# Kernel optimization log

Hardware: AMD Instinct MI355X
Metric: run time of the kernel (lower is better)

Reference implementation:

```python
import jax, jax.numpy as jnp
import numpy as np

N = 50000        # nodes
R = 51           # enriched relations (25 fwd + 25 inverse + self-loop)
F_IN = 32        # feat_size
E = 32           # embed_size
C = 16           # num_classes
B = 30           # num_bases
NNZ = 2_000_000  # nonzeros in vertical adjacency


def _xavier(key, shape):
    # mimics nn.init.xavier_uniform_ with gain for relu (sqrt(2))
    fan_in, fan_out = shape[-2], shape[-1]
    a = np.sqrt(2.0) * np.sqrt(6.0 / (fan_in + fan_out))
    return jax.random.uniform(key, shape, jnp.float32, -a, a)


def setup_inputs() -> dict:
    key = jax.random.key(0)
    ks = jax.random.split(key, 8)
    # COO of vertical adjacency, shape (R*N, N)
    rows = jax.random.randint(ks[0], (NNZ,), 0, R * N)
    cols = jax.random.randint(ks[1], (NNZ,), 0, N)
    # row-normalized values: vals = 1 / row_degree  (sum_sparse with rows=True)
    deg = jax.ops.segment_sum(jnp.ones((NNZ,), jnp.float32), rows, num_segments=R * N)
    vals = (1.0 / jnp.maximum(deg, 1.0))[rows]
    features = jax.random.normal(ks[2], (N, F_IN), jnp.float32)
    comps1 = _xavier(ks[3], (R, B))
    bases1 = _xavier(ks[4], (B, F_IN, E))
    comps2 = _xavier(ks[5], (R, B))
    bases2 = _xavier(ks[6], (B, E, C))
    bias1 = jnp.zeros((E,), jnp.float32)
    bias2 = jnp.zeros((C,), jnp.float32)
    return {
        "features": features, "vals": vals,
        "comps1": comps1, "bases1": bases1, "bias1": bias1,
        "comps2": comps2, "bases2": bases2, "bias2": bias2,
        "rows": rows, "cols": cols,
    }


def _spmm(rows, cols, vals, x):
    # (R*N, N) sparse @ (N, f) dense -> (R*N, f)
    return jax.ops.segment_sum(vals[:, None] * x[cols], rows, num_segments=R * N)


def reference(features, vals, comps1, bases1, bias1, comps2, bases2, bias2, rows, cols):
    # layer 1: SpMM then basis-decomposed per-relation mixing
    h = _spmm(rows, cols, vals, features).reshape(R, N, F_IN)   # (r, n, f)
    w1 = jnp.einsum('rb,bfe->rfe', comps1, bases1)              # (r, f, e)
    h = jnp.einsum('rnf,rfe->ne', h, w1)                        # (n, e)
    h = jax.nn.relu(h + bias1)
    # layer 2
    h = _spmm(rows, cols, vals, h).reshape(R, N, E)             # (r, n, e)
    w2 = jnp.einsum('rb,bho->rho', comps2, bases2)              # (r, e, c)
    h = jnp.einsum('rho,rnh->no', w2, h)                        # (n, c)
    return h + bias2
```

## Files before the change

kernel.cpp:

```cpp
#include <hip/hip_runtime.h>

#define NNODES 50000
#define RREL 51
#define FIN 32
#define EDIM 32
#define CDIM 16
#define BB 30
#define NNZ_ 2000000
#define EPB 4096
#define NBUK 391
#define PCAP_MAX 2750128

typedef unsigned int uint32;
typedef unsigned short ushort;
typedef uint32 u32x2 __attribute__((ext_vector_type(2)));
typedef uint32 u32x4 __attribute__((ext_vector_type(4)));
typedef short bf16x8 __attribute__((ext_vector_type(8)));
typedef float f32x4 __attribute__((ext_vector_type(4)));
typedef float f32x16 __attribute__((ext_vector_type(16)));

static __device__ __forceinline__ uint32 pack_bf16x2(float a, float b) {
    uint32 ua = __builtin_bit_cast(uint32, a);
    uint32 ub = __builtin_bit_cast(uint32, b);
    ua += 0x7fffu + ((ua >> 16) & 1u);
    ub += 0x7fffu + ((ub >> 16) & 1u);
    return (ua >> 16) | (ub & 0xffff0000u);
}
static __device__ __forceinline__ ushort bf16_1(float x) {
    uint32 u = __builtin_bit_cast(uint32, x);
    u += 0x7fffu + ((u >> 16) & 1u);
    return (ushort)(u >> 16);
}

__global__ void k_weights2(const float* __restrict__ bases1, const float* __restrict__ bases2,
                           ushort* __restrict__ Wb1, ushort* __restrict__ Wb2) {
    int i = blockIdx.x * 256 + threadIdx.x;
    if (i < 960 * 32) {
        int e = i & 31, k = i >> 5;
        int b = k >> 5, f = k & 31;
        float v = bases1[b * 1024 + f * 32 + e];
        Wb1[((k >> 3) * 32 + e) * 8 + (k & 7)] = bf16_1(v);
    }
    if (i < 960 * 16) {
        int e = i & 15, k = i >> 4;
        int b = k >> 5, h = k & 31;
        float v = bases2[b * 512 + h * 16 + e];
        Wb2[((k >> 3) * 16 + e) * 8 + (k & 7)] = bf16_1(v);
    }
}

__global__ void k_tobf16(const float2* __restrict__ src, uint32* __restrict__ dst, int n2) {
    int i = blockIdx.x * 256 + threadIdx.x;
    if (i < n2) {
        float2 f = src[i];
        dst[i] = pack_bf16x2(f.x, f.y);
    }
}

__global__ __launch_bounds__(1024) void k_bukhist(const int* __restrict__ rows,
                                                  int* __restrict__ buk_cnt) {
    __shared__ int lc[NBUK];
    int t = threadIdx.x;
    if (t < NBUK) lc[t] = 0;
    __syncthreads();
    size_t k = (size_t)blockIdx.x * EPB + (size_t)t * 4;
    int rr[4];
    if (k + 4 <= NNZ_) {
        int4 rw = *(const int4*)(rows + k);
        rr[0] = rw.x; rr[1] = rw.y; rr[2] = rw.z; rr[3] = rw.w;
    } else {
#pragma unroll
        for (int j = 0; j < 4; j++) rr[j] = (k + j < NNZ_) ? rows[k + j] : -1;
    }
#pragma unroll
    for (int j = 0; j < 4; j++)
        if (rr[j] >= 0) {
            int rel = rr[j] / NNODES;
            int dst = rr[j] - rel * NNODES;
            atomicAdd(&lc[dst >> 7], 1);
        }
    __syncthreads();
    if (t < NBUK) atomicAdd(&buk_cnt[t], lc[t]);
}

__global__ void k_scan1(const int* __restrict__ buk_cnt, int* __restrict__ buk_base,
                        int* __restrict__ buk_cur) {
    if (threadIdx.x == 0) {
        int a = 0;
        for (int b = 0; b < NBUK; b++) { buk_base[b] = a; buk_cur[b] = a; a += buk_cnt[b]; }
        buk_base[NBUK] = a;
    }
}

__global__ __launch_bounds__(1024) void k_bucket2(const int* __restrict__ rows,
                                                  const int* __restrict__ cols,
                                                  const float* __restrict__ vals,
                                                  int* __restrict__ buk_cur,
                                                  u32x2* __restrict__ tok8,
                                                  float* __restrict__ sval_b) {
    __shared__ int bukc[NBUK], lb[NBUK], gb[NBUK];
    __shared__ int ssum[1024];
    __shared__ u32x2 st8[EPB];
    __shared__ float sv[EPB];
    int t = threadIdx.x;
    size_t base = (size_t)blockIdx.x * EPB;
    int total = (int)(((size_t)NNZ_ - base < (size_t)EPB) ? ((size_t)NNZ_ - base) : (size_t)EPB);
    if (t < NBUK) bukc[t] = 0;
    __syncthreads();
    size_t k = base + (size_t)t * 4;
    int bv[4]; uint32 tx[4], ty[4]; float vv[4];
    if (k + 4 <= NNZ_) {
        int4 rw = *(const int4*)(rows + k);
        int4 cw = *(const int4*)(cols + k);
        float4 vw = *(const float4*)(vals + k);
        int rr[4] = {rw.x, rw.y, rw.z, rw.w};
        int cc[4] = {cw.x, cw.y, cw.z, cw.w};
        vv[0] = vw.x; vv[1] = vw.y; vv[2] = vw.z; vv[3] = vw.w;
#pragma unroll
        for (int j = 0; j < 4; j++) {
            int rel = rr[j] / NNODES;
            int dst = rr[j] - rel * NNODES;
            bv[j] = dst >> 7;
            tx[j] = (uint32)dst | ((uint32)rel << 16);
            ty[j] = (uint32)cc[j] | ((uint32)rel << 16);
        }
    } else {
#pragma unroll
        for (int j = 0; j < 4; j++) {
            if (k + j < NNZ_) {
                int r = rows[k + j];
                int rel = r / NNODES;
                int dst = r - rel * NNODES;
                bv[j] = dst >> 7;
                tx[j] = (uint32)dst | ((uint32)rel << 16);
                ty[j] = (uint32)cols[k + j] | ((uint32)rel << 16);
                vv[j] = vals[k + j];
            } else bv[j] = -1;
        }
    }
#pragma unroll
    for (int j = 0; j < 4; j++)
        if (bv[j] >= 0) atomicAdd(&bukc[bv[j]], 1);
    __syncthreads();
    int v = (t < NBUK) ? bukc[t] : 0;
    ssum[t] = v;
    __syncthreads();
    for (int off = 1; off < 1024; off <<= 1) {
        int u = (t >= off) ? ssum[t - off] : 0;
        __syncthreads();
        ssum[t] += u;
        __syncthreads();
    }
    if (t < NBUK) { lb[t] = ssum[t] - v; gb[t] = atomicAdd(&buk_cur[t], v); }
    __syncthreads();
    if (t < NBUK) bukc[t] = 0;
    __syncthreads();
#pragma unroll
    for (int j = 0; j < 4; j++) {
        if (bv[j] >= 0) {
            int slot = lb[bv[j]] + atomicAdd(&bukc[bv[j]], 1);
            u32x2 w; w.x = tx[j]; w.y = ty[j];
            st8[slot] = w;
            sv[slot] = vv[j];
        }
    }
    __syncthreads();
    for (int s = t; s < total; s += 1024) {
        u32x2 w = st8[s];
        int bk = (int)((w.x & 0xFFFFu) >> 7);
        int pos = gb[bk] + (s - lb[bk]);
        tok8[pos] = w;
        sval_b[pos] = sv[s];
    }
}

__global__ __launch_bounds__(256) void k_rank3a(const u32x2* __restrict__ tok8,
                                                const int* __restrict__ buk_base,
                                                int* __restrict__ pbuk_cnt) {
    __shared__ int lcnt[128];
    __shared__ int tot;
    int b = blockIdx.x, t = threadIdx.x;
    if (t < 128) lcnt[t] = 0;
    if (t == 0) tot = 0;
    __syncthreads();
    int lo = buk_base[b], hi = buk_base[b + 1];
    for (int i = lo + t; i < hi; i += 256) atomicAdd(&lcnt[tok8[i].x & 127], 1);
    __syncthreads();
    if (t < 128) atomicAdd(&tot, (lcnt[t] + 15) & ~15);
    __syncthreads();
    if (t == 0) pbuk_cnt[b] = tot;
}

__global__ void k_scan2(const int* __restrict__ pbuk_cnt, int* __restrict__ pbuk_base) {
    if (threadIdx.x == 0) {
        int a = 0;
        for (int b = 0; b < NBUK; b++) { pbuk_base[b] = a; a += pbuk_cnt[b]; }
        pbuk_base[NBUK] = a;
    }
}

__global__ __launch_bounds__(256) void k_place(const u32x2* __restrict__ tok8,
                                               const float* __restrict__ sval_b,
                                               const int* __restrict__ buk_base,
                                               const int* __restrict__ pbuk_base,
                                               int* __restrict__ pdst_base,
                                               uint32* __restrict__ pe_sr,
                                               float* __restrict__ pe_val) {
    __shared__ int lcnt[128], lexc[128], lrank[128], ssc[128];
    int b = blockIdx.x, t = threadIdx.x;
    int lo = buk_base[b], hi = buk_base[b + 1], pb = pbuk_base[b];
    if (t < 128) { lcnt[t] = 0; lrank[t] = 0; }
    __syncthreads();
    for (int i = lo + t; i < hi; i += 256) atomicAdd(&lcnt[tok8[i].x & 127], 1);
    __syncthreads();
    int v = 0;
    if (t < 128) { v = (lcnt[t] + 15) & ~15; ssc[t] = v; }
    __syncthreads();
    for (int off = 1; off < 128; off <<= 1) {
        int u = (t >= off && t < 128) ? ssc[t - off] : 0;
        __syncthreads();
        if (t < 128) ssc[t] += u;
        __syncthreads();
    }
    if (t < 128) {
        lexc[t] = ssc[t] - v;
        int d = (b << 7) + t;
        if (d <= NNODES) pdst_base[d] = pb + lexc[t];
    }
    __syncthreads();
    for (int i = lo + t; i < hi; i += 256) {
        u32x2 w = tok8[i];
        int dl = (int)(w.x & 127u);
        int pos = pb + lexc[dl] + atomicAdd(&lrank[dl], 1);
        pe_sr[pos] = w.y;
        pe_val[pos] = sval_b[i];
    }
    if (t < 128) {
        int s0 = pb + lexc[t] + lcnt[t];
        int s1 = pb + lexc[t] + ((lcnt[t] + 15) & ~15);
        for (int i = s0; i < s1; i++) { pe_sr[i] = 0u; pe_val[i] = 0.f; }
    }
}

template <int FO, bool RELU, bool BF16OUT>
__global__ __launch_bounds__(256) void k_fused(const uint32* __restrict__ pe_sr,
                                               const float* __restrict__ pe_val,
                                               const int* __restrict__ pdst_base,
                                               const u32x4* __restrict__ Xb,
                                               const u32x4* __restrict__ Wb,
                                               const float* __restrict__ comps,
                                               const float* __restrict__ bias,
                                               void* __restrict__ outp) {
    __shared__ ushort comps_lb[RREL * 32];
    __shared__ uint32 eds[4][64];
    __shared__ float edv[4][64];
    __shared__ __align__(16) ushort xst[4][4][512];
    __shared__ __align__(16) ushort ubuf[4][4][968];
    int t = threadIdx.x, lane = t & 63, wv = t >> 6;
    for (int i = t; i < RREL * 32; i += 256) {
        int r = i >> 5, b = i & 31;
        comps_lb[i] = (b < BB) ? bf16_1(comps[r * BB + b]) : (ushort)0;
    }
    __syncthreads();
    int m = lane & 31, hf = lane >> 5, k0 = hf * 8;
    int ln15 = lane & 15, quad = lane >> 4;
    int d0 = (blockIdx.x * 4 + wv) * 8;
    if (d0 >= NNODES) return;

    auto ccprep = [&](int wi) -> u32x4 {
        float cc[8];
#pragma unroll
        for (int j = 0; j < 8; j++) {
            uint32 sr = eds[wv][wi * 16 + k0 + j];
            float vv = edv[wv][wi * 16 + k0 + j];
            uint32 cu = (uint32)comps_lb[((sr >> 16) << 5) | m] << 16;
            cc[j] = vv * __builtin_bit_cast(float, cu);
        }
        u32x4 r = { pack_bf16x2(cc[0], cc[1]), pack_bf16x2(cc[2], cc[3]),
                    pack_bf16x2(cc[4], cc[5]), pack_bf16x2(cc[6], cc[7]) };
        return r;
    };
    auto dowin = [&](int wi, u32x4 avq, f32x16 a) -> f32x16 {
        const ushort* xs = &xst[wv][wi][0];
        uint32 b0 = (uint32)xs[(k0 + 0) * 32 + m] | ((uint32)xs[(k0 + 1) * 32 + m] << 16);
        uint32 b1 = (uint32)xs[(k0 + 2) * 32 + m] | ((uint32)xs[(k0 + 3) * 32 + m] << 16);
        uint32 b2 = (uint32)xs[(k0 + 4) * 32 + m] | ((uint32)xs[(k0 + 5) * 32 + m] << 16);
        uint32 b3 = (uint32)xs[(k0 + 6) * 32 + m] | ((uint32)xs[(k0 + 7) * 32 + m] << 16);
        u32x4 bvq = { b0, b1, b2, b3 };
        return __builtin_amdgcn_mfma_f32_32x32x16_bf16(
            __builtin_bit_cast(bf16x8, avq), __builtin_bit_cast(bf16x8, bvq), a, 0, 0, 0);
    };

    int base0 = pdst_base[d0];
    uint32 pvs = __builtin_nontemporal_load(&pe_sr[base0 + lane]);
    float  pvv = __builtin_nontemporal_load(&pe_val[base0 + lane]);
    u32x4 gx0, gx1, gx2, gx3;
    {
        int s0_ = __shfl((int)pvs, (lane >> 2), 64);
        gx0 = Xb[(size_t)((uint32)s0_ & 0xFFFFu) * 4 + (lane & 3)];
        int s1_ = __shfl((int)pvs, 16 + (lane >> 2), 64);
        gx1 = Xb[(size_t)((uint32)s1_ & 0xFFFFu) * 4 + (lane & 3)];
        int s2_ = __shfl((int)pvs, 32 + (lane >> 2), 64);
        gx2 = Xb[(size_t)((uint32)s2_ & 0xFFFFu) * 4 + (lane & 3)];
        int s3_ = __shfl((int)pvs, 48 + (lane >> 2), 64);
        gx3 = Xb[(size_t)((uint32)s3_ & 0xFFFFu) * 4 + (lane & 3)];
    }

#pragma unroll 1
    for (int batch = 0; batch < 2; batch++) {
        int db = d0 + batch * 4;
#pragma unroll 1
        for (int s = 0; s < 4; s++) {
            int d = db + s;
            int lo = pdst_base[d], segEnd = pdst_base[d + 1];
            f32x16 acc;
#pragma unroll
            for (int i = 0; i < 16; i++) acc[i] = 0.f;
#pragma unroll 1
            for (int c0 = lo; c0 < segEnd; c0 += 64) {
                eds[wv][lane] = pvs;
                edv[wv][lane] = pvv;
                int nxt = c0 + 64; if (nxt > segEnd) nxt = segEnd;
                uint32 npvs = __builtin_nontemporal_load(&pe_sr[nxt + lane]);
                float  npvv = __builtin_nontemporal_load(&pe_val[nxt + lane]);
                int nwin = (segEnd - c0) >> 4;
                if (nwin > 4) nwin = 4;
                u32x4 av0, av1, av2, av3;
                av0 = ccprep(0);
                if (nwin > 1) av1 = ccprep(1);
                if (nwin > 2) av2 = ccprep(2);
                if (nwin > 3) av3 = ccprep(3);
                *(u32x4*)&xst[wv][0][lane * 8] = gx0;
                if (nwin > 1) *(u32x4*)&xst[wv][1][lane * 8] = gx1;
                if (nwin > 2) *(u32x4*)&xst[wv][2][lane * 8] = gx2;
                if (nwin > 3) *(u32x4*)&xst[wv][3][lane * 8] = gx3;
                acc = dowin(0, av0, acc);
                if (nwin > 1) acc = dowin(1, av1, acc);
                if (nwin > 2) acc = dowin(2, av2, acc);
                if (nwin > 3) acc = dowin(3, av3, acc);
                {
                    int s0_ = __shfl((int)npvs, (lane >> 2), 64);
                    gx0 = Xb[(size_t)((uint32)s0_ & 0xFFFFu) * 4 + (lane & 3)];
                    int s1_ = __shfl((int)npvs, 16 + (lane >> 2), 64);
                    gx1 = Xb[(size_t)((uint32)s1_ & 0xFFFFu) * 4 + (lane & 3)];
                    int s2_ = __shfl((int)npvs, 32 + (lane >> 2), 64);
                    gx2 = Xb[(size_t)((uint32)s2_ & 0xFFFFu) * 4 + (lane & 3)];
                    int s3_ = __shfl((int)npvs, 48 + (lane >> 2), 64);
                    gx3 = Xb[(size_t)((uint32)s3_ & 0xFFFFu) * 4 + (lane & 3)];
                }
                pvs = npvs; pvv = npvv;
            }
#pragma unroll
            for (int r = 0; r < 16; r++) {
                int b = (r & 3) + 8 * (r >> 2) + 4 * hf;
                float vme = acc[r];
                float vot = __shfl_xor(vme, 1, 64);
                if (b < BB && !(m & 1)) {
                    *(uint32*)&ubuf[wv][s][b * 32 + m] = pack_bf16x2(vme, vot);
                }
            }
        }
        const int NT = FO / 16;
        f32x4 a2[NT];
#pragma unroll
        for (int tt = 0; tt < NT; tt++)
#pragma unroll
            for (int i = 0; i < 4; i++) a2[tt][i] = 0.f;
#pragma unroll 6
        for (int ks = 0; ks < 30; ks++) {
            bf16x8 af = *(const bf16x8*)&ubuf[wv][ln15 & 3][ks * 32 + quad * 8];
#pragma unroll
            for (int tt = 0; tt < NT; tt++) {
                bf16x8 bf2 = __builtin_bit_cast(bf16x8, Wb[(ks * 4 + quad) * FO + ln15 + 16 * tt]);
                a2[tt] = __builtin_amdgcn_mfma_f32_16x16x32_bf16(af, bf2, a2[tt], 0, 0, 0);
            }
        }
        if (quad == 0) {
#pragma unroll
            for (int r = 0; r < 4; r++) {
                int dst = db + r;
                if (dst < NNODES) {
                    if (BF16OUT) {
                        ushort* hp = (ushort*)outp;
#pragma unroll
                        for (int tt = 0; tt < NT; tt++) {
                            float o = a2[tt][r] + bias[ln15 + 16 * tt];
                            if (RELU) o = fmaxf(o, 0.f);
                            hp[(size_t)dst * FO + ln15 + 16 * tt] = bf16_1(o);
                        }
                    } else {
                        float o = a2[0][r] + bias[ln15];
                        if (RELU) o = fmaxf(o, 0.f);
                        ((float*)outp)[(size_t)dst * FO + ln15] = o;
                    }
                }
            }
        }
    }
}

extern "C" void kernel_launch(void* const* d_in, const int* in_sizes, int n_in,
                              void* d_out, int out_size, void* d_ws, size_t ws_size,
                              hipStream_t stream) {
    const float* features = (const float*)d_in[0];
    const float* vals     = (const float*)d_in[1];
    const float* comps1   = (const float*)d_in[2];
    const float* bases1   = (const float*)d_in[3];
    const float* bias1    = (const float*)d_in[4];
    const float* comps2   = (const float*)d_in[5];
    const float* bases2   = (const float*)d_in[6];
    const float* bias2    = (const float*)d_in[7];
    const int*   rows     = (const int*)d_in[8];
    const int*   cols     = (const int*)d_in[9];
    float* out = (float*)d_out;

    float* ws = (float*)d_ws;
    size_t o = 0;
    ushort* Wb1 = (ushort*)(ws + o); o += 960 * 32 / 2;
    ushort* Wb2 = (ushort*)(ws + o); o += 960 * 16 / 2;
    uint32* Xb  = (uint32*)(ws + o); o += (size_t)NNODES * 16;
    uint32* h1b = (uint32*)(ws + o); o += (size_t)NNODES * 16;
    uint32* pe_sr  = (uint32*)(ws + o); o += PCAP_MAX;
    float*  pe_val = (float*)(ws + o);  o += PCAP_MAX;
    int* pdst_base = (int*)(ws + o); o += NNODES + 8;
    int* buk_cnt   = (int*)(ws + o); o += NBUK;
    int* buk_base  = (int*)(ws + o); o += NBUK + 1;
    int* buk_cur   = (int*)(ws + o); o += NBUK;
    int* pbuk_cnt  = (int*)(ws + o); o += NBUK;
    int* pbuk_base = (int*)(ws + o); o += NBUK + 1;
    o = (o + 1) & ~(size_t)1;
    u32x2* tok8 = (u32x2*)(ws + o); o += 2 * (size_t)NNZ_;
    float* sval_b = (float*)(ws + o); o += (size_t)NNZ_;

    const int NB = (NNZ_ + EPB - 1) / EPB;

    hipMemsetAsync(buk_cnt, 0, NBUK * sizeof(int), stream);

    k_weights2<<<(960 * 32 + 255) / 256, 256, 0, stream>>>(bases1, bases2, Wb1, Wb2);
    k_tobf16<<<(NNODES * FIN / 2 + 255) / 256, 256, 0, stream>>>((const float2*)features, Xb,
                                                                 NNODES * FIN / 2);
    k_bukhist<<<NB, 1024, 0, stream>>>(rows, buk_cnt);
    k_scan1<<<1, 64, 0, stream>>>(buk_cnt, buk_base, buk_cur);
    k_bucket2<<<NB, 1024, 0, stream>>>(rows, cols, vals, buk_cur, tok8, sval_b);
    k_rank3a<<<NBUK, 256, 0, stream>>>(tok8, buk_base, pbuk_cnt);
    k_scan2<<<1, 64, 0, stream>>>(pbuk_cnt, pbuk_base);
    k_place<<<NBUK, 256, 0, stream>>>(tok8, sval_b, buk_base, pbuk_base, pdst_base, pe_sr, pe_val);

    k_fused<EDIM, true, true><<<(NNODES + 31) / 32, 256, 0, stream>>>(
        pe_sr, pe_val, pdst_base, (const u32x4*)Xb, (const u32x4*)Wb1, comps1, bias1, h1b);
    k_fused<CDIM, false, false><<<(NNODES + 31) / 32, 256, 0, stream>>>(
        pe_sr, pe_val, pdst_base, (const u32x4*)h1b, (const u32x4*)Wb2, comps2, bias2, out);
}
```

Before: 361.2 us.

## Scale gathered features by edge value and halve per-wave dst batch

The per-edge normalisation value is now applied to the gathered bf16 feature rows before they are staged in LDS, instead of to the relation-coefficient operand. This removes the edv shared buffer and the per-edge value reads from the ccprep path. Each wave now processes four batches of two destination nodes instead of two batches of four, which halves the ubuf LDS footprint so more blocks may fit per CU. The cost is that the second-stage 16x16 MFMA pass runs twice as often, with fewer useful rows per pass, and the features go through an extra unpack, scale and repack step.

```diff
diff --git a/kernel.cpp b/kernel.cpp
--- a/kernel.cpp
+++ b/kernel.cpp
@@ -253,9 +253,8 @@
                                                void* __restrict__ outp) {
     __shared__ ushort comps_lb[RREL * 32];
     __shared__ uint32 eds[4][64];
-    __shared__ float edv[4][64];
     __shared__ __align__(16) ushort xst[4][4][512];
-    __shared__ __align__(16) ushort ubuf[4][4][968];
+    __shared__ __align__(16) ushort ubuf[4][2][968];
     int t = threadIdx.x, lane = t & 63, wv = t >> 6;
     for (int i = t; i < RREL * 32; i += 256) {
         int r = i >> 5, b = i & 31;
@@ -268,16 +267,24 @@
     if (d0 >= NNODES) return;
 
     auto ccprep = [&](int wi) -> u32x4 {
-        float cc[8];
+        uint32 c[8];
 #pragma unroll
         for (int j = 0; j < 8; j++) {
             uint32 sr = eds[wv][wi * 16 + k0 + j];
-            float vv = edv[wv][wi * 16 + k0 + j];
-            uint32 cu = (uint32)comps_lb[((sr >> 16) << 5) | m] << 16;
-            cc[j] = vv * __builtin_bit_cast(float, cu);
-        }
-        u32x4 r = { pack_bf16x2(cc[0], cc[1]), pack_bf16x2(cc[2], cc[3]),
-                    pack_bf16x2(cc[4], cc[5]), pack_bf16x2(cc[6], cc[7]) };
+            c[j] = (uint32)comps_lb[((sr >> 16) << 5) | m];
+        }
+        u32x4 r = { c[0] | (c[1] << 16), c[2] | (c[3] << 16),
+                    c[4] | (c[5] << 16), c[6] | (c[7] << 16) };
+        return r;
+    };
+    auto scale8 = [&](u32x4 g, float vm) -> u32x4 {
+        u32x4 r;
+#pragma unroll
+        for (int q = 0; q < 4; q++) {
+            float lo = __builtin_bit_cast(float, g[q] << 16) * vm;
+            float hi = __builtin_bit_cast(float, g[q] & 0xffff0000u) * vm;
+            r[q] = pack_bf16x2(lo, hi);
+        }
         return r;
     };
     auto dowin = [&](int wi, u32x4 avq, f32x16 a) -> f32x16 {
@@ -307,10 +314,10 @@
     }
 
 #pragma unroll 1
-    for (int batch = 0; batch < 2; batch++) {
-        int db = d0 + batch * 4;
+    for (int batch = 0; batch < 4; batch++) {
+        int db = d0 + batch * 2;
 #pragma unroll 1
-        for (int s = 0; s < 4; s++) {
+        for (int s = 0; s < 2; s++) {
             int d = db + s;
             int lo = pdst_base[d], segEnd = pdst_base[d + 1];
             f32x16 acc;
@@ -319,7 +326,6 @@
 #pragma unroll 1
             for (int c0 = lo; c0 < segEnd; c0 += 64) {
                 eds[wv][lane] = pvs;
-                edv[wv][lane] = pvv;
                 int nxt = c0 + 64; if (nxt > segEnd) nxt = segEnd;
                 uint32 npvs = __builtin_nontemporal_load(&pe_sr[nxt + lane]);
                 float  npvv = __builtin_nontemporal_load(&pe_val[nxt + lane]);
@@ -330,10 +336,22 @@
                 if (nwin > 1) av1 = ccprep(1);
                 if (nwin > 2) av2 = ccprep(2);
                 if (nwin > 3) av3 = ccprep(3);
-                *(u32x4*)&xst[wv][0][lane * 8] = gx0;
-                if (nwin > 1) *(u32x4*)&xst[wv][1][lane * 8] = gx1;
-                if (nwin > 2) *(u32x4*)&xst[wv][2][lane * 8] = gx2;
-                if (nwin > 3) *(u32x4*)&xst[wv][3][lane * 8] = gx3;
+                {
+                    float vm = __shfl(pvv, (lane >> 2), 64);
+                    *(u32x4*)&xst[wv][0][lane * 8] = scale8(gx0, vm);
+                }
+                if (nwin > 1) {
+                    float vm = __shfl(pvv, 16 + (lane >> 2), 64);
+                    *(u32x4*)&xst[wv][1][lane * 8] = scale8(gx1, vm);
+                }
+                if (nwin > 2) {
+                    float vm = __shfl(pvv, 32 + (lane >> 2), 64);
+                    *(u32x4*)&xst[wv][2][lane * 8] = scale8(gx2, vm);
+                }
+                if (nwin > 3) {
+                    float vm = __shfl(pvv, 48 + (lane >> 2), 64);
+                    *(u32x4*)&xst[wv][3][lane * 8] = scale8(gx3, vm);
+                }
                 acc = dowin(0, av0, acc);
                 if (nwin > 1) acc = dowin(1, av1, acc);
                 if (nwin > 2) acc = dowin(2, av2, acc);
@@ -368,7 +386,7 @@
             for (int i = 0; i < 4; i++) a2[tt][i] = 0.f;
 #pragma unroll 6
         for (int ks = 0; ks < 30; ks++) {
-            bf16x8 af = *(const bf16x8*)&ubuf[wv][ln15 & 3][ks * 32 + quad * 8];
+            bf16x8 af = *(const bf16x8*)&ubuf[wv][ln15 & 1][ks * 32 + quad * 8];
 #pragma unroll
             for (int tt = 0; tt < NT; tt++) {
                 bf16x8 bf2 = __builtin_bit_cast(bf16x8, Wb[(ks * 4 + quad) * FO + ln15 + 16 * tt]);
@@ -377,7 +395,7 @@
         }
         if (quad == 0) {
 #pragma unroll
-            for (int r = 0; r < 4; r++) {
+            for (int r = 0; r < 2; r++) {
                 int dst = db + r;
                 if (dst < NNODES) {
                     if (BF16OUT) {
```

Result: slower. 381.4 us (+5.6%).

## Replace two-level bucket sort with direct per-destination counting sort via global atomics

Applied to the files above, without the earlier changes.

Replaces the bucket histogram, bucket scatter, rank and place pipeline with a direct per-destination histogram in global atomics, a per-bucket padded-size scan, and a single scatter pass that places each edge using a global atomic cursor per destination. This drops the intermediate tok8/sval_b arrays and their extra read/write passes, and also parallelises the bucket scan with wave shuffles. Empty destinations now get a 16-slot padded segment, so the padding capacity grows. The cost is heavy contention on global atomics (two million atomics on 50k counters, done twice) and random scattered writes.

```diff
diff --git a/kernel.cpp b/kernel.cpp
--- a/kernel.cpp
+++ b/kernel.cpp
@@ -9,7 +9,7 @@
 #define NNZ_ 2000000
 #define EPB 4096
 #define NBUK 391
-#define PCAP_MAX 2750128
+#define PCAP_MAX 2800128
 
 typedef unsigned int uint32;
 typedef unsigned short ushort;
@@ -57,188 +57,123 @@
     }
 }
 
-__global__ __launch_bounds__(1024) void k_bukhist(const int* __restrict__ rows,
-                                                  int* __restrict__ buk_cnt) {
-    __shared__ int lc[NBUK];
-    int t = threadIdx.x;
-    if (t < NBUK) lc[t] = 0;
-    __syncthreads();
-    size_t k = (size_t)blockIdx.x * EPB + (size_t)t * 4;
-    int rr[4];
+__global__ __launch_bounds__(1024) void k_dsthist(const int* __restrict__ rows,
+                                                  int* __restrict__ dst_cnt) {
+    size_t k = (size_t)blockIdx.x * EPB + (size_t)threadIdx.x * 4;
     if (k + 4 <= NNZ_) {
         int4 rw = *(const int4*)(rows + k);
-        rr[0] = rw.x; rr[1] = rw.y; rr[2] = rw.z; rr[3] = rw.w;
+        int rr[4] = {rw.x, rw.y, rw.z, rw.w};
+#pragma unroll
+        for (int j = 0; j < 4; j++) {
+            int rel = rr[j] / NNODES;
+            atomicAdd(&dst_cnt[rr[j] - rel * NNODES], 1);
+        }
     } else {
-#pragma unroll
-        for (int j = 0; j < 4; j++) rr[j] = (k + j < NNZ_) ? rows[k + j] : -1;
-    }
-#pragma unroll
-    for (int j = 0; j < 4; j++)
-        if (rr[j] >= 0) {
-            int rel = rr[j] / NNODES;
-            int dst = rr[j] - rel * NNODES;
-            atomicAdd(&lc[dst >> 7], 1);
-        }
+        for (int j = 0; j < 4; j++)
+            if (k + j < NNZ_) {
+                int r = rows[k + j];
+                int rel = r / NNODES;
+                atomicAdd(&dst_cnt[r - rel * NNODES], 1);
+            }
+    }
+}
+
+__global__ __launch_bounds__(128) void k_pb(const int* __restrict__ dst_cnt,
+                                            int* __restrict__ pbuk_cnt) {
+    __shared__ int tot;
+    int b = blockIdx.x, t = threadIdx.x;
+    if (t == 0) tot = 0;
     __syncthreads();
-    if (t < NBUK) atomicAdd(&buk_cnt[t], lc[t]);
-}
-
-__global__ void k_scan1(const int* __restrict__ buk_cnt, int* __restrict__ buk_base,
-                        int* __restrict__ buk_cur) {
-    if (threadIdx.x == 0) {
-        int a = 0;
-        for (int b = 0; b < NBUK; b++) { buk_base[b] = a; buk_cur[b] = a; a += buk_cnt[b]; }
-        buk_base[NBUK] = a;
-    }
-}
-
-__global__ __launch_bounds__(1024) void k_bucket2(const int* __restrict__ rows,
-                                                  const int* __restrict__ cols,
-                                                  const float* __restrict__ vals,
-                                                  int* __restrict__ buk_cur,
-                                                  u32x2* __restrict__ tok8,
-                                                  float* __restrict__ sval_b) {
-    __shared__ int bukc[NBUK], lb[NBUK], gb[NBUK];
-    __shared__ int ssum[1024];
-    __shared__ u32x2 st8[EPB];
-    __shared__ float sv[EPB];
+    int d = (b << 7) + t;
+    int v = 0;
+    if (d < NNODES) {
+        int c = dst_cnt[d];
+        v = (c + 15) & ~15;
+        if (v == 0) v = 16;
+    }
+    atomicAdd(&tot, v);
+    __syncthreads();
+    if (t == 0) pbuk_cnt[b] = tot;
+}
+
+__global__ void k_scan2(const int* __restrict__ pbuk_cnt, int* __restrict__ pbuk_base) {
     int t = threadIdx.x;
-    size_t base = (size_t)blockIdx.x * EPB;
-    int total = (int)(((size_t)NNZ_ - base < (size_t)EPB) ? ((size_t)NNZ_ - base) : (size_t)EPB);
-    if (t < NBUK) bukc[t] = 0;
+    int carry = 0;
+    for (int c = 0; c < NBUK; c += 64) {
+        int idx = c + t;
+        int v = (idx < NBUK) ? pbuk_cnt[idx] : 0;
+        int sum = v;
+#pragma unroll
+        for (int off = 1; off < 64; off <<= 1) {
+            int u = __shfl_up(sum, off, 64);
+            if (t >= off) sum += u;
+        }
+        if (idx < NBUK) pbuk_base[idx] = carry + sum - v;
+        carry += __shfl(sum, 63, 64);
+    }
+    if (t == 0) pbuk_base[NBUK] = carry;
+}
+
+__global__ __launch_bounds__(128) void k_base(const int* __restrict__ dst_cnt,
+                                              const int* __restrict__ pbuk_base,
+                                              int* __restrict__ pdst_base,
+                                              uint32* __restrict__ pe_sr,
+                                              float* __restrict__ pe_val) {
+    __shared__ int ssc[128];
+    int b = blockIdx.x, t = threadIdx.x;
+    int d = (b << 7) + t;
+    int cnt = (d < NNODES) ? dst_cnt[d] : 0;
+    int v = 0;
+    if (d < NNODES) {
+        v = (cnt + 15) & ~15;
+        if (v == 0) v = 16;
+    }
+    ssc[t] = v;
     __syncthreads();
-    size_t k = base + (size_t)t * 4;
-    int bv[4]; uint32 tx[4], ty[4]; float vv[4];
+    for (int off = 1; off < 128; off <<= 1) {
+        int u = (t >= off) ? ssc[t - off] : 0;
+        __syncthreads();
+        ssc[t] += u;
+        __syncthreads();
+    }
+    int base = pbuk_base[b] + ssc[t] - v;
+    if (d <= NNODES + 4) pdst_base[d] = base;
+    for (int i = base + cnt; i < base + v; i++) { pe_sr[i] = 0u; pe_val[i] = 0.f; }
+}
+
+__global__ __launch_bounds__(1024) void k_placeD(const int* __restrict__ rows,
+                                                 const int* __restrict__ cols,
+                                                 const float* __restrict__ vals,
+                                                 const int* __restrict__ pdst_base,
+                                                 int* __restrict__ dst_cur,
+                                                 uint32* __restrict__ pe_sr,
+                                                 float* __restrict__ pe_val) {
+    size_t k = (size_t)blockIdx.x * EPB + (size_t)threadIdx.x * 4;
     if (k + 4 <= NNZ_) {
         int4 rw = *(const int4*)(rows + k);
         int4 cw = *(const int4*)(cols + k);
         float4 vw = *(const float4*)(vals + k);
         int rr[4] = {rw.x, rw.y, rw.z, rw.w};
         int cc[4] = {cw.x, cw.y, cw.z, cw.w};
-        vv[0] = vw.x; vv[1] = vw.y; vv[2] = vw.z; vv[3] = vw.w;
+        float vv[4] = {vw.x, vw.y, vw.z, vw.w};
 #pragma unroll
         for (int j = 0; j < 4; j++) {
             int rel = rr[j] / NNODES;
             int dst = rr[j] - rel * NNODES;
-            bv[j] = dst >> 7;
-            tx[j] = (uint32)dst | ((uint32)rel << 16);
-            ty[j] = (uint32)cc[j] | ((uint32)rel << 16);
+            int pos = pdst_base[dst] + atomicAdd(&dst_cur[dst], 1);
+            pe_sr[pos] = (uint32)cc[j] | ((uint32)rel << 16);
+            pe_val[pos] = vv[j];
         }
     } else {
-#pragma unroll
-        for (int j = 0; j < 4; j++) {
+        for (int j = 0; j < 4; j++)
             if (k + j < NNZ_) {
                 int r = rows[k + j];
                 int rel = r / NNODES;
                 int dst = r - rel * NNODES;
-                bv[j] = dst >> 7;
-                tx[j] = (uint32)dst | ((uint32)rel << 16);
-                ty[j] = (uint32)cols[k + j] | ((uint32)rel << 16);
-                vv[j] = vals[k + j];
-            } else bv[j] = -1;
-        }
-    }
-#pragma unroll
-    for (int j = 0; j < 4; j++)
-        if (bv[j] >= 0) atomicAdd(&bukc[bv[j]], 1);
-    __syncthreads();
-    int v = (t < NBUK) ? bukc[t] : 0;
-    ssum[t] = v;
-    __syncthreads();
-    for (int off = 1; off < 1024; off <<= 1) {
-        int u = (t >= off) ? ssum[t - off] : 0;
-        __syncthreads();
-        ssum[t] += u;
-        __syncthreads();
-    }
-    if (t < NBUK) { lb[t] = ssum[t] - v; gb[t] = atomicAdd(&buk_cur[t], v); }
-    __syncthreads();
-    if (t < NBUK) bukc[t] = 0;
-    __syncthreads();
-#pragma unroll
-    for (int j = 0; j < 4; j++) {
-        if (bv[j] >= 0) {
-            int slot = lb[bv[j]] + atomicAdd(&bukc[bv[j]], 1);
-            u32x2 w; w.x = tx[j]; w.y = ty[j];
-            st8[slot] = w;
-            sv[slot] = vv[j];
-        }
-    }
-    __syncthreads();
-    for (int s = t; s < total; s += 1024) {
-        u32x2 w = st8[s];
-        int bk = (int)((w.x & 0xFFFFu) >> 7);
-        int pos = gb[bk] + (s - lb[bk]);
-        tok8[pos] = w;
-        sval_b[pos] = sv[s];
-    }
-}
-
-__global__ __launch_bounds__(256) void k_rank3a(const u32x2* __restrict__ tok8,
-                                                const int* __restrict__ buk_base,
-                                                int* __restrict__ pbuk_cnt) {
-    __shared__ int lcnt[128];
-    __shared__ int tot;
-    int b = blockIdx.x, t = threadIdx.x;
-    if (t < 128) lcnt[t] = 0;
-    if (t == 0) tot = 0;
-    __syncthreads();
-    int lo = buk_base[b], hi = buk_base[b + 1];
-    for (int i = lo + t; i < hi; i += 256) atomicAdd(&lcnt[tok8[i].x & 127], 1);
-    __syncthreads();
-    if (t < 128) atomicAdd(&tot, (lcnt[t] + 15) & ~15);
-    __syncthreads();
-    if (t == 0) pbuk_cnt[b] = tot;
-}
-
-__global__ void k_scan2(const int* __restrict__ pbuk_cnt, int* __restrict__ pbuk_base) {
-    if (threadIdx.x == 0) {
-        int a = 0;
-        for (int b = 0; b < NBUK; b++) { pbuk_base[b] = a; a += pbuk_cnt[b]; }
-        pbuk_base[NBUK] = a;
-    }
-}
-
-__global__ __launch_bounds__(256) void k_place(const u32x2* __restrict__ tok8,
-                                               const float* __restrict__ sval_b,
-                                               const int* __restrict__ buk_base,
-                                               const int* __restrict__ pbuk_base,
-                                               int* __restrict__ pdst_base,
-                                               uint32* __restrict__ pe_sr,
-                                               float* __restrict__ pe_val) {
-    __shared__ int lcnt[128], lexc[128], lrank[128], ssc[128];
-    int b = blockIdx.x, t = threadIdx.x;
-    int lo = buk_base[b], hi = buk_base[b + 1], pb = pbuk_base[b];
-    if (t < 128) { lcnt[t] = 0; lrank[t] = 0; }
-    __syncthreads();
-    for (int i = lo + t; i < hi; i += 256) atomicAdd(&lcnt[tok8[i].x & 127], 1);
-    __syncthreads();
-    int v = 0;
-    if (t < 128) { v = (lcnt[t] + 15) & ~15; ssc[t] = v; }
-    __syncthreads();
-    for (int off = 1; off < 128; off <<= 1) {
-        int u = (t >= off && t < 128) ? ssc[t - off] : 0;
-        __syncthreads();
-        if (t < 128) ssc[t] += u;
-        __syncthreads();
-    }
-    if (t < 128) {
-        lexc[t] = ssc[t] - v;
-        int d = (b << 7) + t;
-        if (d <= NNODES) pdst_base[d] = pb + lexc[t];
-    }
-    __syncthreads();
-    for (int i = lo + t; i < hi; i += 256) {
-        u32x2 w = tok8[i];
-        int dl = (int)(w.x & 127u);
-        int pos = pb + lexc[dl] + atomicAdd(&lrank[dl], 1);
-        pe_sr[pos] = w.y;
-        pe_val[pos] = sval_b[i];
-    }
-    if (t < 128) {
-        int s0 = pb + lexc[t] + lcnt[t];
-        int s1 = pb + lexc[t] + ((lcnt[t] + 15) & ~15);
-        for (int i = s0; i < s1; i++) { pe_sr[i] = 0u; pe_val[i] = 0.f; }
+                int pos = pdst_base[dst] + atomicAdd(&dst_cur[dst], 1);
+                pe_sr[pos] = (uint32)cols[k + j] | ((uint32)rel << 16);
+                pe_val[pos] = vals[k + j];
+            }
     }
 }
 
@@ -423,28 +358,23 @@
     uint32* pe_sr  = (uint32*)(ws + o); o += PCAP_MAX;
     float*  pe_val = (float*)(ws + o);  o += PCAP_MAX;
     int* pdst_base = (int*)(ws + o); o += NNODES + 8;
-    int* buk_cnt   = (int*)(ws + o); o += NBUK;
-    int* buk_base  = (int*)(ws + o); o += NBUK + 1;
-    int* buk_cur   = (int*)(ws + o); o += NBUK;
+    int* dst_cnt   = (int*)(ws + o); o += NNODES;
+    int* dst_cur   = (int*)(ws + o); o += NNODES;
     int* pbuk_cnt  = (int*)(ws + o); o += NBUK;
     int* pbuk_base = (int*)(ws + o); o += NBUK + 1;
-    o = (o + 1) & ~(size_t)1;
-    u32x2* tok8 = (u32x2*)(ws + o); o += 2 * (size_t)NNZ_;
-    float* sval_b = (float*)(ws + o); o += (size_t)NNZ_;
 
     const int NB = (NNZ_ + EPB - 1) / EPB;
 
-    hipMemsetAsync(buk_cnt, 0, NBUK * sizeof(int), stream);
+    hipMemsetAsync(dst_cnt, 0, 2 * NNODES * sizeof(int), stream);
 
     k_weights2<<<(960 * 32 + 255) / 256, 256, 0, stream>>>(bases1, bases2, Wb1, Wb2);
     k_tobf16<<<(NNODES * FIN / 2 + 255) / 256, 256, 0, stream>>>((const float2*)features, Xb,
                                                                  NNODES * FIN / 2);
-    k_bukhist<<<NB, 1024, 0, stream>>>(rows, buk_cnt);
-    k_scan1<<<1, 64, 0, stream>>>(buk_cnt, buk_base, buk_cur);
-    k_bucket2<<<NB, 1024, 0, stream>>>(rows, cols, vals, buk_cur, tok8, sval_b);
-    k_rank3a<<<NBUK, 256, 0, stream>>>(tok8, buk_base, pbuk_cnt);
+    k_dsthist<<<NB, 1024, 0, stream>>>(rows, dst_cnt);
+    k_pb<<<NBUK, 128, 0, stream>>>(dst_cnt, pbuk_cnt);
     k_scan2<<<1, 64, 0, stream>>>(pbuk_cnt, pbuk_base);
-    k_place<<<NBUK, 256, 0, stream>>>(tok8, sval_b, buk_base, pbuk_base, pdst_base, pe_sr, pe_val);
+    k_base<<<NBUK, 128, 0, stream>>>(dst_cnt, pbuk_base, pdst_base, pe_sr, pe_val);
+    k_placeD<<<NB, 1024, 0, stream>>>(rows, cols, vals, pdst_base, dst_cur, pe_sr, pe_val);
 
     k_fused<EDIM, true, true><<<(NNODES + 31) / 32, 256, 0, stream>>>(
         pe_sr, pe_val, pdst_base, (const u32x4*)Xb, (const u32x4*)Wb1, comps1, bias1, h1b);
```

Measured after the change: 517.9 us. 1.43x slower.

## Compute per-destination counts in histogram pass and split placement into base/scatter kernels

Applied to the files above, without the earlier changes.

The histogram kernel now also atomically counts edges per destination node in global memory. That removes the extra pass over tok8 that k_rank3a and k_place used to recount destinations per bucket. Padding offsets now come from a new k_base kernel, which also zeroes the pad slots, and k_place2 does only the scatter. Both serial single-thread scans become wave-level shuffle scans. The cost is two million global atomics into a 50K-entry array and one extra launch, and every destination now gets at least 16 padded slots, so PCAP_MAX is raised.

```diff
diff --git a/kernel.cpp b/kernel.cpp
--- a/kernel.cpp
+++ b/kernel.cpp
@@ -9,7 +9,7 @@
 #define NNZ_ 2000000
 #define EPB 4096
 #define NBUK 391
-#define PCAP_MAX 2750128
+#define PCAP_MAX 2800128
 
 typedef unsigned int uint32;
 typedef unsigned short ushort;
@@ -57,8 +57,9 @@
     }
 }
 
-__global__ __launch_bounds__(1024) void k_bukhist(const int* __restrict__ rows,
-                                                  int* __restrict__ buk_cnt) {
+__global__ __launch_bounds__(1024) void k_hist(const int* __restrict__ rows,
+                                               int* __restrict__ buk_cnt,
+                                               int* __restrict__ dst_cnt) {
     __shared__ int lc[NBUK];
     int t = threadIdx.x;
     if (t < NBUK) lc[t] = 0;
@@ -78,6 +79,7 @@
             int rel = rr[j] / NNODES;
             int dst = rr[j] - rel * NNODES;
             atomicAdd(&lc[dst >> 7], 1);
+            atomicAdd(&dst_cnt[dst], 1);
         }
     __syncthreads();
     if (t < NBUK) atomicAdd(&buk_cnt[t], lc[t]);
@@ -85,11 +87,22 @@
 
 __global__ void k_scan1(const int* __restrict__ buk_cnt, int* __restrict__ buk_base,
                         int* __restrict__ buk_cur) {
-    if (threadIdx.x == 0) {
-        int a = 0;
-        for (int b = 0; b < NBUK; b++) { buk_base[b] = a; buk_cur[b] = a; a += buk_cnt[b]; }
-        buk_base[NBUK] = a;
-    }
+    int t = threadIdx.x;
+    int carry = 0;
+    for (int c = 0; c < NBUK; c += 64) {
+        int idx = c + t;
+        int v = (idx < NBUK) ? buk_cnt[idx] : 0;
+        int sum = v;
+#pragma unroll
+        for (int off = 1; off < 64; off <<= 1) {
+            int u = __shfl_up(sum, off, 64);
+            if (t >= off) sum += u;
+        }
+        int exc = carry + sum - v;
+        if (idx < NBUK) { buk_base[idx] = exc; buk_cur[idx] = exc; }
+        carry += __shfl(sum, 63, 64);
+    }
+    if (t == 0) buk_base[NBUK] = carry;
 }
 
 __global__ __launch_bounds__(1024) void k_bucket2(const int* __restrict__ rows,
@@ -174,71 +187,88 @@
     }
 }
 
-__global__ __launch_bounds__(256) void k_rank3a(const u32x2* __restrict__ tok8,
-                                                const int* __restrict__ buk_base,
-                                                int* __restrict__ pbuk_cnt) {
-    __shared__ int lcnt[128];
+__global__ __launch_bounds__(128) void k_pb(const int* __restrict__ dst_cnt,
+                                            int* __restrict__ pbuk_cnt) {
     __shared__ int tot;
     int b = blockIdx.x, t = threadIdx.x;
-    if (t < 128) lcnt[t] = 0;
     if (t == 0) tot = 0;
     __syncthreads();
+    int d = (b << 7) + t;
+    int v = 0;
+    if (d < NNODES) {
+        int c = dst_cnt[d];
+        v = (c + 15) & ~15;
+        if (v == 0) v = 16;
+    }
+    atomicAdd(&tot, v);
+    __syncthreads();
+    if (t == 0) pbuk_cnt[b] = tot;
+}
+
+__global__ void k_scan2(const int* __restrict__ pbuk_cnt, int* __restrict__ pbuk_base) {
+    int t = threadIdx.x;
+    int carry = 0;
+    for (int c = 0; c < NBUK; c += 64) {
+        int idx = c + t;
+        int v = (idx < NBUK) ? pbuk_cnt[idx] : 0;
+        int sum = v;
+#pragma unroll
+        for (int off = 1; off < 64; off <<= 1) {
+            int u = __shfl_up(sum, off, 64);
+            if (t >= off) sum += u;
+        }
+        if (idx < NBUK) pbuk_base[idx] = carry + sum - v;
+        carry += __shfl(sum, 63, 64);
+    }
+    if (t == 0) pbuk_base[NBUK] = carry;
+}
+
+__global__ __launch_bounds__(128) void k_base(const int* __restrict__ dst_cnt,
+                                              const int* __restrict__ pbuk_base,
+                                              int* __restrict__ pdst_base,
+                                              uint32* __restrict__ pe_sr,
+                                              float* __restrict__ pe_val) {
+    __shared__ int ssc[128];
+    int b = blockIdx.x, t = threadIdx.x;
+    int d = (b << 7) + t;
+    int cnt = (d < NNODES) ? dst_cnt[d] : 0;
+    int v = 0;
+    if (d < NNODES) {
+        v = (cnt + 15) & ~15;
+        if (v == 0) v = 16;
+    }
+    ssc[t] = v;
+    __syncthreads();
+    for (int off = 1; off < 128; off <<= 1) {
+        int u = (t >= off) ? ssc[t - off] : 0;
+        __syncthreads();
+        ssc[t] += u;
+        __syncthreads();
+    }
+    int base = pbuk_base[b] + ssc[t] - v;
+    if (d <= NNODES + 4) pdst_base[d] = base;
+    for (int i = base + cnt; i < base + v; i++) { pe_sr[i] = 0u; pe_val[i] = 0.f; }
+}
+
+__global__ __launch_bounds__(256) void k_place2(const u32x2* __restrict__ tok8,
+                                                const float* __restrict__ sval_b,
+                                                const int* __restrict__ buk_base,
+                                                const int* __restrict__ pdst_base,
+                                                uint32* __restrict__ pe_sr,
+                                                float* __restrict__ pe_val) {
+    __shared__ int lrank[128];
+    int b = blockIdx.x, t = threadIdx.x;
+    if (t < 128) lrank[t] = 0;
+    __syncthreads();
     int lo = buk_base[b], hi = buk_base[b + 1];
-    for (int i = lo + t; i < hi; i += 256) atomicAdd(&lcnt[tok8[i].x & 127], 1);
-    __syncthreads();
-    if (t < 128) atomicAdd(&tot, (lcnt[t] + 15) & ~15);
-    __syncthreads();
-    if (t == 0) pbuk_cnt[b] = tot;
-}
-
-__global__ void k_scan2(const int* __restrict__ pbuk_cnt, int* __restrict__ pbuk_base) {
-    if (threadIdx.x == 0) {
-        int a = 0;
-        for (int b = 0; b < NBUK; b++) { pbuk_base[b] = a; a += pbuk_cnt[b]; }
-        pbuk_base[NBUK] = a;
-    }
-}
-
-__global__ __launch_bounds__(256) void k_place(const u32x2* __restrict__ tok8,
-                                               const float* __restrict__ sval_b,
-                                               const int* __restrict__ buk_base,
-                                               const int* __restrict__ pbuk_base,
-                                               int* __restrict__ pdst_base,
-                                               uint32* __restrict__ pe_sr,
-                                               float* __restrict__ pe_val) {
-    __shared__ int lcnt[128], lexc[128], lrank[128], ssc[128];
-    int b = blockIdx.x, t = threadIdx.x;
-    int lo = buk_base[b], hi = buk_base[b + 1], pb = pbuk_base[b];
-    if (t < 128) { lcnt[t] = 0; lrank[t] = 0; }
-    __syncthreads();
-    for (int i = lo + t; i < hi; i += 256) atomicAdd(&lcnt[tok8[i].x & 127], 1);
-    __syncthreads();
-    int v = 0;
-    if (t < 128) { v = (lcnt[t] + 15) & ~15; ssc[t] = v; }
-    __syncthreads();
-    for (int off = 1; off < 128; off <<= 1) {
-        int u = (t >= off && t < 128) ? ssc[t - off] : 0;
-        __syncthreads();
-        if (t < 128) ssc[t] += u;
-        __syncthreads();
-    }
-    if (t < 128) {
-        lexc[t] = ssc[t] - v;
-        int d = (b << 7) + t;
-        if (d <= NNODES) pdst_base[d] = pb + lexc[t];
-    }
-    __syncthreads();
+    int d0 = b << 7;
     for (int i = lo + t; i < hi; i += 256) {
         u32x2 w = tok8[i];
+        float v = sval_b[i];
         int dl = (int)(w.x & 127u);
-        int pos = pb + lexc[dl] + atomicAdd(&lrank[dl], 1);
+        int pos = pdst_base[d0 + dl] + atomicAdd(&lrank[dl], 1);
         pe_sr[pos] = w.y;
-        pe_val[pos] = sval_b[i];
-    }
-    if (t < 128) {
-        int s0 = pb + lexc[t] + lcnt[t];
-        int s1 = pb + lexc[t] + ((lcnt[t] + 15) & ~15);
-        for (int i = s0; i < s1; i++) { pe_sr[i] = 0u; pe_val[i] = 0.f; }
+        pe_val[pos] = v;
     }
 }
 
@@ -423,6 +453,7 @@
     uint32* pe_sr  = (uint32*)(ws + o); o += PCAP_MAX;
     float*  pe_val = (float*)(ws + o);  o += PCAP_MAX;
     int* pdst_base = (int*)(ws + o); o += NNODES + 8;
+    int* dst_cnt   = (int*)(ws + o); o += NNODES;
     int* buk_cnt   = (int*)(ws + o); o += NBUK;
     int* buk_base  = (int*)(ws + o); o += NBUK + 1;
     int* buk_cur   = (int*)(ws + o); o += NBUK;
@@ -434,17 +465,18 @@
 
     const int NB = (NNZ_ + EPB - 1) / EPB;
 
-    hipMemsetAsync(buk_cnt, 0, NBUK * sizeof(int), stream);
+    hipMemsetAsync(dst_cnt, 0, (NNODES + NBUK) * sizeof(int), stream);
 
     k_weights2<<<(960 * 32 + 255) / 256, 256, 0, stream>>>(bases1, bases2, Wb1, Wb2);
     k_tobf16<<<(NNODES * FIN / 2 + 255) / 256, 256, 0, stream>>>((const float2*)features, Xb,
                                                                  NNODES * FIN / 2);
-    k_bukhist<<<NB, 1024, 0, stream>>>(rows, buk_cnt);
+    k_hist<<<NB, 1024, 0, stream>>>(rows, buk_cnt, dst_cnt);
     k_scan1<<<1, 64, 0, stream>>>(buk_cnt, buk_base, buk_cur);
     k_bucket2<<<NB, 1024, 0, stream>>>(rows, cols, vals, buk_cur, tok8, sval_b);
-    k_rank3a<<<NBUK, 256, 0, stream>>>(tok8, buk_base, pbuk_cnt);
+    k_pb<<<NBUK, 128, 0, stream>>>(dst_cnt, pbuk_cnt);
     k_scan2<<<1, 64, 0, stream>>>(pbuk_cnt, pbuk_base);
-    k_place<<<NBUK, 256, 0, stream>>>(tok8, sval_b, buk_base, pbuk_base, pdst_base, pe_sr, pe_val);
+    k_base<<<NBUK, 128, 0, stream>>>(dst_cnt, pbuk_base, pdst_base, pe_sr, pe_val);
+    k_place2<<<NBUK, 256, 0, stream>>>(tok8, sval_b, buk_base, pdst_base, pe_sr, pe_val);
 
     k_fused<EDIM, true, true><<<(NNODES + 31) / 32, 256, 0, stream>>>(
         pe_sr, pe_val, pdst_base, (const u32x4*)Xb, (const u32x4*)Wb1, comps1, bias1, h1b);
```

Measured after the change: 424.4 us. 17.5% more time.
